# Kernel optimization log

Measured on AMD Instinct MI355X. Metric: run time of the kernel, lower is better.

The kernel has to match this reference:

```python
import jax, jax.numpy as jnp
import numpy as np
import math

N = 100000
E = 800000
H = 256
TDIM = 32
NTYPES = 22
NLAYERS = 2


def layer_norm(x, g, b, eps=1e-5):
    mu = jnp.mean(x, axis=-1, keepdims=True)
    var = jnp.var(x, axis=-1, keepdims=True)
    return (x - mu) * jax.lax.rsqrt(var + eps) * g + b


def setup_inputs() -> dict:
    key = jax.random.key(0)
    ks = jax.random.split(key, 16)
    s = 1.0 / math.sqrt(H)
    inp = {
        "clause_reprs": jax.random.normal(ks[0], (N, H), dtype=jnp.float32),
        "timestamps": jax.random.uniform(ks[1], (N,), dtype=jnp.float32) * 10000.0,
        "deriv_types": jax.random.randint(ks[2], (N,), 0, NTYPES),
        "derivation_edges": jax.random.randint(ks[3], (2, E), 0, N),
        # params
        "emb_table": jax.random.normal(ks[4], (NTYPES, H), dtype=jnp.float32),
        "temp_W": jax.random.normal(ks[5], (TDIM, H), dtype=jnp.float32) / math.sqrt(TDIM),
        "temp_b": jnp.zeros((H,), jnp.float32),
        "fus_W1": jax.random.normal(ks[6], (3 * H, H), dtype=jnp.float32) / math.sqrt(3 * H),
        "fus_b1": jnp.zeros((H,), jnp.float32),
        "fus_W2": jax.random.normal(ks[7], (H, H), dtype=jnp.float32) * s,
        "fus_b2": jnp.zeros((H,), jnp.float32),
        "in_g": jnp.ones((H,), jnp.float32),
        "in_b": jnp.zeros((H,), jnp.float32),
        "deriv_W": jax.random.normal(ks[8], (NLAYERS, 2 * H, H), dtype=jnp.float32) / math.sqrt(2 * H),
        "deriv_b": jnp.zeros((NLAYERS, H), jnp.float32),
        "dn_g": jnp.ones((NLAYERS, H), jnp.float32),
        "dn_b": jnp.zeros((NLAYERS, H), jnp.float32),
    }
    return inp


def reference(clause_reprs, timestamps, deriv_types, derivation_edges,
              emb_table, temp_W, temp_b, fus_W1, fus_b1, fus_W2, fus_b2,
              in_g, in_b, deriv_W, deriv_b, dn_g, dn_b):
    # --- temporal sinusoidal encoding -> projection ---
    half = TDIM // 2
    freqs = jnp.exp(-math.log(10000.0) * jnp.arange(half, dtype=jnp.float32) / half)
    angles = timestamps[:, None] * freqs[None, :]                      # (N, half)
    pe = jnp.concatenate([jnp.sin(angles), jnp.cos(angles)], axis=-1)  # (N, TDIM)
    temporal_enc = pe @ temp_W + temp_b                                # (N, H)
    # --- derivation type embedding ---
    deriv_enc = emb_table[deriv_types]                                 # (N, H)
    # --- input fusion + residual + LN ---
    cat = jnp.concatenate([clause_reprs, temporal_enc, deriv_enc], axis=-1)
    fused = jax.nn.relu(cat @ fus_W1 + fus_b1) @ fus_W2 + fus_b2
    x = layer_norm(fused + clause_reprs, in_g, in_b)
    # --- derivation message passing along DAG edges (parent -> child) ---
    src, dst = derivation_edges[0], derivation_edges[1]
    count = jnp.zeros((N, 1), jnp.float32).at[dst].add(1.0)
    count = jnp.maximum(count, 1.0)
    for l in range(NLAYERS):
        parent_msgs = x[src]                                           # (E, H) gather
        agg = jnp.zeros_like(x).at[dst].add(parent_msgs) / count       # (N, H) scatter-add
        combined = jnp.concatenate([x, agg], axis=-1)                  # (N, 2H)
        update = jax.nn.relu(combined @ deriv_W[l] + deriv_b[l])
        x = layer_norm(x + update, dn_g[l], dn_b[l])
    return x
```

## Files before the change

### kernel.cpp

```cpp
#include <hip/hip_runtime.h>
#include <hip/hip_bf16.h>
#include <math.h>

#define N_NODES 100000
#define N_EDGES 800000
#define H 256
#define NTYPES 22
#define SCAN_G 98
#define GRID_G ((N_NODES + 63) / 64)

typedef __attribute__((ext_vector_type(8))) short short8;
typedef __attribute__((ext_vector_type(4))) float f32x4;
typedef unsigned short u16;

__device__ __forceinline__ u16 f2bf(float f) {
    unsigned u = __float_as_uint(f);
    u += 0x7FFF + ((u >> 16) & 1);
    return (u16)(u >> 16);
}
__device__ __forceinline__ float bf2f(u16 u) {
    return __uint_as_float(((unsigned)u) << 16);
}

__global__ __launch_bounds__(256) void prep_small(
    const float* __restrict__ temp_W, const float* __restrict__ temp_b,
    const float* __restrict__ emb, const float* __restrict__ fus_W1,
    const float* __restrict__ fus_b1,
    float* __restrict__ C1, float* __restrict__ C2, float* __restrict__ beff)
{
    int b = blockIdx.x;
    int j = threadIdx.x;
    if (b < 32) {
        float acc = 0.f;
        #pragma unroll 8
        for (int m = 0; m < H; ++m)
            acc += temp_W[b * H + m] * fus_W1[(size_t)(H + m) * H + j];
        C1[b * H + j] = acc;
    } else if (b < 32 + NTYPES) {
        int e = b - 32;
        float acc = 0.f;
        #pragma unroll 8
        for (int m = 0; m < H; ++m)
            acc += emb[e * H + m] * fus_W1[(size_t)(2 * H + m) * H + j];
        C2[e * H + j] = acc;
    } else {
        float acc = fus_b1[j];
        #pragma unroll 8
        for (int m = 0; m < H; ++m)
            acc += temp_b[m] * fus_W1[(size_t)(H + m) * H + j];
        beff[j] = acc;
    }
}

__global__ __launch_bounds__(256) void prep_frag(
    const float* __restrict__ fus_W1, const float* __restrict__ C1,
    const float* __restrict__ fus_W2, const float* __restrict__ deriv_W,
    u16* __restrict__ wblob)
{
    int s = blockIdx.x;
    const float* src; int kbase;
    if (s < 8)       { src = fus_W1;              kbase = s * 32; }
    else if (s == 8) { src = C1;                  kbase = 0; }
    else if (s < 17) { src = fus_W2;              kbase = (s - 9) * 32; }
    else if (s < 33) { src = deriv_W;             kbase = (s - 17) * 32; }
    else             { src = deriv_W + 512 * H;   kbase = (s - 33) * 32; }
    #pragma unroll
    for (int it = 0; it < 4; ++it) {
        int c = it * 256 + threadIdx.x;
        int l = c & 63, nt = c >> 6;
        int n = (nt << 4) | (l & 15);
        int k0 = kbase + ((l >> 4) << 3);
        short8 v;
        #pragma unroll
        for (int i = 0; i < 8; ++i)
            v[i] = (short)f2bf(src[(size_t)(k0 + i) * H + n]);
        *reinterpret_cast<short8*>(wblob + (size_t)s * 8192 + (size_t)c * 8) = v;
    }
}

__global__ void count_kernel(const int* __restrict__ dst, int* __restrict__ cnt)
{
    int e = blockIdx.x * blockDim.x + threadIdx.x;
    if (e < N_EDGES) atomicAdd(&cnt[dst[e]], 1);
}

__global__ __launch_bounds__(1024) void scan1_kernel(
    const int* __restrict__ cnt, int* __restrict__ off, int* __restrict__ bsum)
{
    __shared__ int s[1024];
    int i = blockIdx.x * 1024 + threadIdx.x;
    int v = (i < N_NODES) ? cnt[i] : 0;
    s[threadIdx.x] = v;
    __syncthreads();
    #pragma unroll
    for (int o = 1; o < 1024; o <<= 1) {
        int t = (threadIdx.x >= o) ? s[threadIdx.x - o] : 0;
        __syncthreads();
        s[threadIdx.x] += t;
        __syncthreads();
    }
    if (i < N_NODES) off[i] = s[threadIdx.x];
    if (threadIdx.x == 1023) bsum[blockIdx.x] = s[1023];
}

__global__ void scan2_kernel(const int* __restrict__ bsum, int* __restrict__ bbase)
{
    if (threadIdx.x == 0) {
        int acc = 0;
        for (int b = 0; b < SCAN_G; ++b) { bbase[b] = acc; acc += bsum[b]; }
    }
}

__global__ __launch_bounds__(1024) void scan3_kernel(
    int* __restrict__ off, const int* __restrict__ bbase,
    const int* __restrict__ cnt, int* __restrict__ cursor)
{
    int i = blockIdx.x * 1024 + threadIdx.x;
    if (i < N_NODES) {
        int incl = off[i] + bbase[blockIdx.x];
        off[i] = incl;
        cursor[i] = incl - cnt[i];
    }
}

__global__ void fill_kernel(const int* __restrict__ src, const int* __restrict__ dst,
                            int* __restrict__ cursor, int* __restrict__ csr)
{
    int e = blockIdx.x * blockDim.x + threadIdx.x;
    if (e < N_EDGES) {
        int pos = atomicAdd(&cursor[dst[e]], 1);
        csr[pos] = src[e];
    }
}

__global__ __launch_bounds__(256) void gather_kernel(
    const u16* __restrict__ xb, const int* __restrict__ csr,
    const int* __restrict__ off, const int* __restrict__ cnt,
    u16* __restrict__ agg)
{
    int node = blockIdx.x * 4 + (threadIdx.x >> 6);
    int l = threadIdx.x & 63;
    int deg = cnt[node];
    int start = off[node] - deg;
    float a0 = 0.f, a1 = 0.f, a2 = 0.f, a3 = 0.f;
    float b0 = 0.f, b1 = 0.f, b2 = 0.f, b3 = 0.f;
    int j = 0;
    for (; j + 1 < deg; j += 2) {
        int s0 = csr[start + j], s1 = csr[start + j + 1];
        ushort4 v0 = *reinterpret_cast<const ushort4*>(xb + (size_t)s0 * H + l * 4);
        ushort4 v1 = *reinterpret_cast<const ushort4*>(xb + (size_t)s1 * H + l * 4);
        a0 += bf2f(v0.x); a1 += bf2f(v0.y); a2 += bf2f(v0.z); a3 += bf2f(v0.w);
        b0 += bf2f(v1.x); b1 += bf2f(v1.y); b2 += bf2f(v1.z); b3 += bf2f(v1.w);
    }
    if (j < deg) {
        int s0 = csr[start + j];
        ushort4 v0 = *reinterpret_cast<const ushort4*>(xb + (size_t)s0 * H + l * 4);
        a0 += bf2f(v0.x); a1 += bf2f(v0.y); a2 += bf2f(v0.z); a3 += bf2f(v0.w);
    }
    float sc = 1.0f / fmaxf((float)deg, 1.0f);
    ushort4 o;
    o.x = f2bf((a0 + b0) * sc); o.y = f2bf((a1 + b1) * sc);
    o.z = f2bf((a2 + b2) * sc); o.w = f2bf((a3 + b3) * sc);
    *reinterpret_cast<ushort4*>(agg + (size_t)node * H + l * 4) = o;
}

__device__ __forceinline__ void stageA_bf16(u16* Af, const u16* __restrict__ src,
                                            int i0, int kbase, int tid)
{
    int w = tid >> 6, l = tid & 63;
    int row = i0 + ((w << 4) | (l & 15));
    row = min(row, N_NODES - 1);
    const u16* p = src + (size_t)row * H + kbase + ((l >> 4) << 3);
    short8 v = *reinterpret_cast<const short8*>(p);
    *reinterpret_cast<short8*>(Af + (size_t)((w << 6) | l) * 8) = v;
}

__device__ __forceinline__ void stageA_f32(u16* Af, const float* __restrict__ src,
                                           int i0, int kbase, int tid)
{
    int w = tid >> 6, l = tid & 63;
    int row = i0 + ((w << 4) | (l & 15));
    row = min(row, N_NODES - 1);
    const float* p = src + (size_t)row * H + kbase + ((l >> 4) << 3);
    float4 a = *reinterpret_cast<const float4*>(p);
    float4 b = *reinterpret_cast<const float4*>(p + 4);
    short8 v;
    v[0] = (short)f2bf(a.x); v[1] = (short)f2bf(a.y);
    v[2] = (short)f2bf(a.z); v[3] = (short)f2bf(a.w);
    v[4] = (short)f2bf(b.x); v[5] = (short)f2bf(b.y);
    v[6] = (short)f2bf(b.z); v[7] = (short)f2bf(b.w);
    *reinterpret_cast<short8*>(Af + (size_t)((w << 6) | l) * 8) = v;
}

__device__ __forceinline__ void stageB(u16* Bf, const u16* __restrict__ wk, int tid)
{
    #pragma unroll
    for (int it = 0; it < 4; ++it) {
        int c = (it << 8) + tid;
        short8 v = *reinterpret_cast<const short8*>(wk + (size_t)c * 8);
        *reinterpret_cast<short8*>(Bf + (size_t)c * 8) = v;
    }
}

__device__ __forceinline__ void mfma_step(const u16* Af, const u16* Bf,
                                          int w, int l, f32x4 acc[4][4])
{
    short8 a[4];
    #pragma unroll
    for (int m = 0; m < 4; ++m)
        a[m] = *reinterpret_cast<const short8*>(Af + (size_t)((m << 6) | l) * 8);
    #pragma unroll
    for (int n = 0; n < 4; ++n) {
        short8 b = *reinterpret_cast<const short8*>(
            Bf + (size_t)((((w << 2) | n) << 6) | l) * 8);
        #pragma unroll
        for (int m = 0; m < 4; ++m)
            acc[m][n] = __builtin_amdgcn_mfma_f32_16x16x32_bf16(a[m], b, acc[m][n],
                                                                0, 0, 0);
    }
}

__global__ __launch_bounds__(256, 3) void k1_mfma(
    const float* __restrict__ clause, const float* __restrict__ ts,
    const int* __restrict__ types, const u16* __restrict__ wblob,
    const float* __restrict__ C2, const float* __restrict__ beff,
    u16* __restrict__ hb)
{
    __shared__ __align__(16) u16 Af[2048];
    __shared__ __align__(16) u16 Bf[8192];
    int tid = threadIdx.x, w = tid >> 6, l = tid & 63;
    int i0 = blockIdx.x * 64;
    f32x4 acc[4][4] = {};

    for (int t = 0; t < 9; ++t) {
        if (t < 8) {
            stageA_f32(Af, clause, i0, t * 32, tid);
        } else {
            int rl = (w << 4) | (l & 15);
            int row = min(i0 + rl, N_NODES - 1);
            float tsv = ts[row];
            int g = l >> 4;
            short8 v;
            #pragma unroll
            for (int i = 0; i < 8; ++i) {
                int k = (g << 3) + i;
                float fr = expf(-0.57564627324851f * (float)(k & 15));
                float ang = tsv * fr;
                float pv = (k < 16) ? sinf(ang) : cosf(ang);
                v[i] = (short)f2bf(pv);
            }
            *reinterpret_cast<short8*>(Af + (size_t)((w << 6) | l) * 8) = v;
        }
        stageB(Bf, wblob + (size_t)t * 8192, tid);
        __syncthreads();
        mfma_step(Af, Bf, w, l, acc);
        __syncthreads();
    }

    int g = l >> 4, c0 = l & 15;
    float be[4];
    #pragma unroll
    for (int n = 0; n < 4; ++n) be[n] = beff[(w << 6) | (n << 4) | c0];
    #pragma unroll
    for (int m = 0; m < 4; ++m) {
        #pragma unroll
        for (int r = 0; r < 4; ++r) {
            int row = i0 + (m << 4) + (g << 2) + r;
            bool ok = row < N_NODES;
            int tp = types[ok ? row : 0];
            const float* c2r = C2 + (size_t)tp * H;
            #pragma unroll
            for (int n = 0; n < 4; ++n) {
                int col = (w << 6) | (n << 4) | c0;
                float val = fmaxf(acc[m][n][r] + be[n] + c2r[col], 0.f);
                if (ok) hb[(size_t)row * H + col] = f2bf(val);
            }
        }
    }
}

__global__ __launch_bounds__(256, 3) void k2_mfma(
    const u16* __restrict__ hb, const u16* __restrict__ wblob,
    const float* __restrict__ b2, const float* __restrict__ clause,
    const float* __restrict__ gW, const float* __restrict__ bW,
    float* __restrict__ xo, u16* __restrict__ xb)
{
    __shared__ __align__(16) u16 Af[2048];
    __shared__ __align__(16) u16 Bf[8192];
    __shared__ float2 red[256];
    int tid = threadIdx.x, w = tid >> 6, l = tid & 63;
    int i0 = blockIdx.x * 64;
    f32x4 acc[4][4] = {};

    for (int t = 0; t < 8; ++t) {
        stageA_bf16(Af, hb, i0, t * 32, tid);
        stageB(Bf, wblob + (size_t)t * 8192, tid);
        __syncthreads();
        mfma_step(Af, Bf, w, l, acc);
        __syncthreads();
    }

    int g = l >> 4, c0 = l & 15;
    float bv[4], gv[4], bbv[4];
    #pragma unroll
    for (int n = 0; n < 4; ++n) {
        int col = (w << 6) | (n << 4) | c0;
        bv[n] = b2[col]; gv[n] = gW[col]; bbv[n] = bW[col];
    }
    #pragma unroll
    for (int m = 0; m < 4; ++m) {
        #pragma unroll
        for (int r = 0; r < 4; ++r) {
            int row = i0 + (m << 4) + (g << 2) + r;
            int rowc = min(row, N_NODES - 1);
            const float* cr = clause + (size_t)rowc * H;
            float s = 0.f, q = 0.f;
            #pragma unroll
            for (int n = 0; n < 4; ++n) {
                float pv = acc[m][n][r] + bv[n] + cr[(w << 6) | (n << 4) | c0];
                acc[m][n][r] = pv;
                s += pv; q += pv * pv;
            }
            #pragma unroll
            for (int o = 1; o < 16; o <<= 1) {
                s += __shfl_xor(s, o);
                q += __shfl_xor(q, o);
            }
            if (c0 == 0)
                red[((m << 4) + (g << 2) + r) * 4 + w] = make_float2(s, q);
        }
    }
    __syncthreads();
    #pragma unroll
    for (int m = 0; m < 4; ++m) {
        #pragma unroll
        for (int r = 0; r < 4; ++r) {
            int rl = (m << 4) + (g << 2) + r;
            int row = i0 + rl;
            float2 t0 = red[rl * 4 + 0], t1 = red[rl * 4 + 1];
            float2 t2 = red[rl * 4 + 2], t3 = red[rl * 4 + 3];
            float S = t0.x + t1.x + t2.x + t3.x;
            float Q = t0.y + t1.y + t2.y + t3.y;
            float mu = S * (1.0f / 256.0f);
            float rstd = rsqrtf(Q * (1.0f / 256.0f) - mu * mu + 1e-5f);
            if (row < N_NODES) {
                #pragma unroll
                for (int n = 0; n < 4; ++n) {
                    int col = (w << 6) | (n << 4) | c0;
                    float val = (acc[m][n][r] - mu) * rstd * gv[n] + bbv[n];
                    xo[(size_t)row * H + col] = val;
                    xb[(size_t)row * H + col] = f2bf(val);
                }
            }
        }
    }
}

template<bool WB16>
__global__ __launch_bounds__(256, 3) void k5_mfma(
    const u16* __restrict__ xb, const u16* __restrict__ aggb,
    float* __restrict__ x, const u16* __restrict__ wblob,
    const float* __restrict__ bl, const float* __restrict__ gl,
    const float* __restrict__ bnl, u16* __restrict__ xbout)
{
    __shared__ __align__(16) u16 Af[2048];
    __shared__ __align__(16) u16 Bf[8192];
    __shared__ float2 red[256];
    int tid = threadIdx.x, w = tid >> 6, l = tid & 63;
    int i0 = blockIdx.x * 64;
    f32x4 acc[4][4] = {};

    for (int t = 0; t < 16; ++t) {
        const u16* src = (t < 8) ? xb : aggb;
        stageA_bf16(Af, src, i0, (t & 7) * 32, tid);
        stageB(Bf, wblob + (size_t)t * 8192, tid);
        __syncthreads();
        mfma_step(Af, Bf, w, l, acc);
        __syncthreads();
    }

    int g = l >> 4, c0 = l & 15;
    float bv[4], gv[4], bbv[4];
    #pragma unroll
    for (int n = 0; n < 4; ++n) {
        int col = (w << 6) | (n << 4) | c0;
        bv[n] = bl[col]; gv[n] = gl[col]; bbv[n] = bnl[col];
    }
    #pragma unroll
    for (int m = 0; m < 4; ++m) {
        #pragma unroll
        for (int r = 0; r < 4; ++r) {
            int row = i0 + (m << 4) + (g << 2) + r;
            int rowc = min(row, N_NODES - 1);
            const float* xr = x + (size_t)rowc * H;
            float s = 0.f, q = 0.f;
            #pragma unroll
            for (int n = 0; n < 4; ++n) {
                float pv = xr[(w << 6) | (n << 4) | c0]
                         + fmaxf(acc[m][n][r] + bv[n], 0.f);
                acc[m][n][r] = pv;
                s += pv; q += pv * pv;
            }
            #pragma unroll
            for (int o = 1; o < 16; o <<= 1) {
                s += __shfl_xor(s, o);
                q += __shfl_xor(q, o);
            }
            if (c0 == 0)
                red[((m << 4) + (g << 2) + r) * 4 + w] = make_float2(s, q);
        }
    }
    __syncthreads();
    #pragma unroll
    for (int m = 0; m < 4; ++m) {
        #pragma unroll
        for (int r = 0; r < 4; ++r) {
            int rl = (m << 4) + (g << 2) + r;
            int row = i0 + rl;
            float2 t0 = red[rl * 4 + 0], t1 = red[rl * 4 + 1];
            float2 t2 = red[rl * 4 + 2], t3 = red[rl * 4 + 3];
            float S = t0.x + t1.x + t2.x + t3.x;
            float Q = t0.y + t1.y + t2.y + t3.y;
            float mu = S * (1.0f / 256.0f);
            float rstd = rsqrtf(Q * (1.0f / 256.0f) - mu * mu + 1e-5f);
            if (row < N_NODES) {
                #pragma unroll
                for (int n = 0; n < 4; ++n) {
                    int col = (w << 6) | (n << 4) | c0;
                    float val = (acc[m][n][r] - mu) * rstd * gv[n] + bbv[n];
                    x[(size_t)row * H + col] = val;
                    if (WB16) xbout[(size_t)row * H + col] = f2bf(val);
                }
            }
        }
    }
}

extern "C" void kernel_launch(void* const* d_in, const int* in_sizes, int n_in,
                              void* d_out, int out_size, void* d_ws, size_t ws_size,
                              hipStream_t stream)
{
    const float* clause  = (const float*)d_in[0];
    const float* ts      = (const float*)d_in[1];
    const int*   types   = (const int*)  d_in[2];
    const int*   edges   = (const int*)  d_in[3];
    const float* emb     = (const float*)d_in[4];
    const float* temp_W  = (const float*)d_in[5];
    const float* temp_b  = (const float*)d_in[6];
    const float* fus_W1  = (const float*)d_in[7];
    const float* fus_b1  = (const float*)d_in[8];
    const float* fus_W2  = (const float*)d_in[9];
    const float* fus_b2  = (const float*)d_in[10];
    const float* in_g    = (const float*)d_in[11];
    const float* in_b    = (const float*)d_in[12];
    const float* deriv_W = (const float*)d_in[13];
    const float* deriv_b = (const float*)d_in[14];
    const float* dn_g    = (const float*)d_in[15];
    const float* dn_b    = (const float*)d_in[16];

    char* p = (char*)d_ws;
    float* C1   = (float*)p;            p += 32 * H * 4;
    float* C2   = (float*)p;            p += NTYPES * H * 4;
    float* beff = (float*)p;            p += H * 4;
    int* cnt    = (int*)p;              p += N_NODES * 4;
    int* off    = (int*)p;              p += N_NODES * 4;
    int* cursor = (int*)p;              p += N_NODES * 4;
    int* bsum   = (int*)p;              p += 128 * 4;
    int* bbase  = (int*)p;              p += 128 * 4;
    int* csr    = (int*)p;              p += N_EDGES * 4;
    u16* wblob  = (u16*)p;              p += 49 * 8192 * 2;
    u16* xb16   = (u16*)p;              p += (size_t)N_NODES * H * 2;
    u16* aggb16 = (u16*)p;              p += (size_t)N_NODES * H * 2;
    float* x    = (float*)d_out;

    const int* src = edges;
    const int* dst = edges + N_EDGES;

    prep_small<<<32 + NTYPES + 1, 256, 0, stream>>>(temp_W, temp_b, emb, fus_W1,
                                                    fus_b1, C1, C2, beff);
    prep_frag<<<49, 256, 0, stream>>>(fus_W1, C1, fus_W2, deriv_W, wblob);

    hipMemsetAsync(cnt, 0, N_NODES * sizeof(int), stream);
    count_kernel<<<(N_EDGES + 255) / 256, 256, 0, stream>>>(dst, cnt);
    scan1_kernel<<<SCAN_G, 1024, 0, stream>>>(cnt, off, bsum);
    scan2_kernel<<<1, 64, 0, stream>>>(bsum, bbase);
    scan3_kernel<<<SCAN_G, 1024, 0, stream>>>(off, bbase, cnt, cursor);
    fill_kernel<<<(N_EDGES + 255) / 256, 256, 0, stream>>>(src, dst, cursor, csr);

    k1_mfma<<<GRID_G, 256, 0, stream>>>(clause, ts, types, wblob, C2, beff, xb16);
    k2_mfma<<<GRID_G, 256, 0, stream>>>(xb16, wblob + (size_t)9 * 8192, fus_b2,
                                        clause, in_g, in_b, x, xb16);

    gather_kernel<<<N_NODES / 4, 256, 0, stream>>>(xb16, csr, off, cnt, aggb16);
    k5_mfma<true><<<GRID_G, 256, 0, stream>>>(
        xb16, aggb16, x, wblob + (size_t)17 * 8192,
        deriv_b, dn_g, dn_b, xb16);
    gather_kernel<<<N_NODES / 4, 256, 0, stream>>>(xb16, csr, off, cnt, aggb16);
    k5_mfma<false><<<GRID_G, 256, 0, stream>>>(
        xb16, aggb16, x, wblob + (size_t)33 * 8192,
        deriv_b + H, dn_g + H, dn_b + H, nullptr);
}
```

Baseline: 546.4 us.

## Fuse input MLP kernels via LDS, use direct-to-LDS loads, drop fp32 residual

Merges the two input-fusion GEMM kernels into one, so the ReLU hidden activations stay in a swizzled LDS buffer and no longer round-trip through global memory. Weight tiles (and A tiles in the layer kernels) are now fetched with global_load_lds direct-to-LDS loads instead of going through registers. The layer kernels process two K-chunks per barrier pair at higher occupancy. The fp32 x intermediate is no longer written; the residual is read back from the bf16 copy, with fp32 written only in the final layer. This cuts memory traffic and synchronisation but lowers residual precision and raises LDS use in the fused kernel.

```diff
diff --git a/kernel.cpp b/kernel.cpp
--- a/kernel.cpp
+++ b/kernel.cpp
@@ -20,6 +20,12 @@
 }
 __device__ __forceinline__ float bf2f(u16 u) {
     return __uint_as_float(((unsigned)u) << 16);
+}
+
+__device__ __forceinline__ void gload16(const void* g, void* l) {
+    __builtin_amdgcn_global_load_lds(
+        (const __attribute__((address_space(1))) unsigned int*)g,
+        (__attribute__((address_space(3))) unsigned int*)l, 16, 0, 0);
 }
 
 __global__ __launch_bounds__(256) void prep_small(
@@ -164,44 +170,6 @@
     *reinterpret_cast<ushort4*>(agg + (size_t)node * H + l * 4) = o;
 }
 
-__device__ __forceinline__ void stageA_bf16(u16* Af, const u16* __restrict__ src,
-                                            int i0, int kbase, int tid)
-{
-    int w = tid >> 6, l = tid & 63;
-    int row = i0 + ((w << 4) | (l & 15));
-    row = min(row, N_NODES - 1);
-    const u16* p = src + (size_t)row * H + kbase + ((l >> 4) << 3);
-    short8 v = *reinterpret_cast<const short8*>(p);
-    *reinterpret_cast<short8*>(Af + (size_t)((w << 6) | l) * 8) = v;
-}
-
-__device__ __forceinline__ void stageA_f32(u16* Af, const float* __restrict__ src,
-                                           int i0, int kbase, int tid)
-{
-    int w = tid >> 6, l = tid & 63;
-    int row = i0 + ((w << 4) | (l & 15));
-    row = min(row, N_NODES - 1);
-    const float* p = src + (size_t)row * H + kbase + ((l >> 4) << 3);
-    float4 a = *reinterpret_cast<const float4*>(p);
-    float4 b = *reinterpret_cast<const float4*>(p + 4);
-    short8 v;
-    v[0] = (short)f2bf(a.x); v[1] = (short)f2bf(a.y);
-    v[2] = (short)f2bf(a.z); v[3] = (short)f2bf(a.w);
-    v[4] = (short)f2bf(b.x); v[5] = (short)f2bf(b.y);
-    v[6] = (short)f2bf(b.z); v[7] = (short)f2bf(b.w);
-    *reinterpret_cast<short8*>(Af + (size_t)((w << 6) | l) * 8) = v;
-}
-
-__device__ __forceinline__ void stageB(u16* Bf, const u16* __restrict__ wk, int tid)
-{
-    #pragma unroll
-    for (int it = 0; it < 4; ++it) {
-        int c = (it << 8) + tid;
-        short8 v = *reinterpret_cast<const short8*>(wk + (size_t)c * 8);
-        *reinterpret_cast<short8*>(Bf + (size_t)c * 8) = v;
-    }
-}
-
 __device__ __forceinline__ void mfma_step(const u16* Af, const u16* Bf,
                                           int w, int l, f32x4 acc[4][4])
 {
@@ -220,30 +188,40 @@
     }
 }
 
-__global__ __launch_bounds__(256, 3) void k1_mfma(
+__global__ __launch_bounds__(256, 3) void k12_mfma(
     const float* __restrict__ clause, const float* __restrict__ ts,
     const int* __restrict__ types, const u16* __restrict__ wblob,
     const float* __restrict__ C2, const float* __restrict__ beff,
-    u16* __restrict__ hb)
+    const float* __restrict__ b2, const float* __restrict__ gW,
+    const float* __restrict__ bW, u16* __restrict__ xb)
 {
     __shared__ __align__(16) u16 Af[2048];
     __shared__ __align__(16) u16 Bf[8192];
+    __shared__ __align__(16) u16 hs[16384];
     int tid = threadIdx.x, w = tid >> 6, l = tid & 63;
+    int g = l >> 4, c0 = l & 15;
     int i0 = blockIdx.x * 64;
+    int rowA = min(i0 + ((w << 4) | c0), N_NODES - 1);
+    int kcol = g << 3;
     f32x4 acc[4][4] = {};
 
     for (int t = 0; t < 9; ++t) {
         if (t < 8) {
-            stageA_f32(Af, clause, i0, t * 32, tid);
+            const float* p = clause + (size_t)rowA * H + t * 32 + kcol;
+            float4 a = *reinterpret_cast<const float4*>(p);
+            float4 b = *reinterpret_cast<const float4*>(p + 4);
+            short8 v;
+            v[0] = (short)f2bf(a.x); v[1] = (short)f2bf(a.y);
+            v[2] = (short)f2bf(a.z); v[3] = (short)f2bf(a.w);
+            v[4] = (short)f2bf(b.x); v[5] = (short)f2bf(b.y);
+            v[6] = (short)f2bf(b.z); v[7] = (short)f2bf(b.w);
+            *reinterpret_cast<short8*>(Af + (size_t)((w << 6) | l) * 8) = v;
         } else {
-            int rl = (w << 4) | (l & 15);
-            int row = min(i0 + rl, N_NODES - 1);
-            float tsv = ts[row];
-            int g = l >> 4;
+            float tsv = ts[rowA];
             short8 v;
             #pragma unroll
             for (int i = 0; i < 8; ++i) {
-                int k = (g << 3) + i;
+                int k = kcol + i;
                 float fr = expf(-0.57564627324851f * (float)(k & 15));
                 float ang = tsv * fr;
                 float pv = (k < 16) ? sinf(ang) : cosf(ang);
@@ -251,56 +229,73 @@
             }
             *reinterpret_cast<short8*>(Af + (size_t)((w << 6) | l) * 8) = v;
         }
-        stageB(Bf, wblob + (size_t)t * 8192, tid);
+        #pragma unroll
+        for (int it = 0; it < 4; ++it) {
+            int c = (it << 8) + tid;
+            gload16(wblob + (size_t)t * 8192 + (size_t)c * 8, Bf + (size_t)c * 8);
+        }
         __syncthreads();
         mfma_step(Af, Bf, w, l, acc);
         __syncthreads();
     }
 
-    int g = l >> 4, c0 = l & 15;
-    float be[4];
-    #pragma unroll
-    for (int n = 0; n < 4; ++n) be[n] = beff[(w << 6) | (n << 4) | c0];
-    #pragma unroll
-    for (int m = 0; m < 4; ++m) {
-        #pragma unroll
-        for (int r = 0; r < 4; ++r) {
-            int row = i0 + (m << 4) + (g << 2) + r;
-            bool ok = row < N_NODES;
-            int tp = types[ok ? row : 0];
-            const float* c2r = C2 + (size_t)tp * H;
-            #pragma unroll
-            for (int n = 0; n < 4; ++n) {
-                int col = (w << 6) | (n << 4) | c0;
-                float val = fmaxf(acc[m][n][r] + be[n] + c2r[col], 0.f);
-                if (ok) hb[(size_t)row * H + col] = f2bf(val);
-            }
-        }
-    }
-}
-
-__global__ __launch_bounds__(256, 3) void k2_mfma(
-    const u16* __restrict__ hb, const u16* __restrict__ wblob,
-    const float* __restrict__ b2, const float* __restrict__ clause,
-    const float* __restrict__ gW, const float* __restrict__ bW,
-    float* __restrict__ xo, u16* __restrict__ xb)
-{
-    __shared__ __align__(16) u16 Af[2048];
-    __shared__ __align__(16) u16 Bf[8192];
-    __shared__ float2 red[256];
-    int tid = threadIdx.x, w = tid >> 6, l = tid & 63;
-    int i0 = blockIdx.x * 64;
-    f32x4 acc[4][4] = {};
+    {
+        float bev[4];
+        #pragma unroll
+        for (int n = 0; n < 4; ++n) bev[n] = beff[(w << 6) | (n << 4) | c0];
+        #pragma unroll
+        for (int m = 0; m < 4; ++m) {
+            #pragma unroll
+            for (int r = 0; r < 4; ++r) {
+                int rl = (m << 4) + (g << 2) + r;
+                int tp = types[min(i0 + rl, N_NODES - 1)];
+                const float* c2r = C2 + (size_t)tp * H;
+                #pragma unroll
+                for (int n = 0; n < 4; ++n) {
+                    int col = (w << 6) | (n << 4) | c0;
+                    float val = fmaxf(acc[m][n][r] + bev[n] + c2r[col], 0.f);
+                    hs[((rl << 8) + col) ^ ((rl & 7) << 3)] = f2bf(val);
+                }
+            }
+        }
+    }
+    __syncthreads();
+
+    #pragma unroll
+    for (int m = 0; m < 4; ++m)
+        #pragma unroll
+        for (int n = 0; n < 4; ++n)
+            acc[m][n] = (f32x4){0.f, 0.f, 0.f, 0.f};
 
     for (int t = 0; t < 8; ++t) {
-        stageA_bf16(Af, hb, i0, t * 32, tid);
-        stageB(Bf, wblob + (size_t)t * 8192, tid);
-        __syncthreads();
-        mfma_step(Af, Bf, w, l, acc);
-        __syncthreads();
-    }
-
-    int g = l >> 4, c0 = l & 15;
+        #pragma unroll
+        for (int it = 0; it < 4; ++it) {
+            int c = (it << 8) + tid;
+            gload16(wblob + (size_t)(9 + t) * 8192 + (size_t)c * 8,
+                    Bf + (size_t)c * 8);
+        }
+        __syncthreads();
+        short8 a[4];
+        int colb = (t << 5) + kcol;
+        #pragma unroll
+        for (int m = 0; m < 4; ++m) {
+            int rl2 = (m << 4) | c0;
+            a[m] = *reinterpret_cast<const short8*>(
+                &hs[((rl2 << 8) + colb) ^ ((c0 & 7) << 3)]);
+        }
+        #pragma unroll
+        for (int n = 0; n < 4; ++n) {
+            short8 b = *reinterpret_cast<const short8*>(
+                Bf + (size_t)((((w << 2) | n) << 6) | l) * 8);
+            #pragma unroll
+            for (int m = 0; m < 4; ++m)
+                acc[m][n] = __builtin_amdgcn_mfma_f32_16x16x32_bf16(a[m], b,
+                                                                    acc[m][n], 0, 0, 0);
+        }
+        __syncthreads();
+    }
+
+    float2* red = reinterpret_cast<float2*>(Af);
     float bv[4], gv[4], bbv[4];
     #pragma unroll
     for (int n = 0; n < 4; ++n) {
@@ -311,8 +306,8 @@
     for (int m = 0; m < 4; ++m) {
         #pragma unroll
         for (int r = 0; r < 4; ++r) {
-            int row = i0 + (m << 4) + (g << 2) + r;
-            int rowc = min(row, N_NODES - 1);
+            int rl = (m << 4) + (g << 2) + r;
+            int rowc = min(i0 + rl, N_NODES - 1);
             const float* cr = clause + (size_t)rowc * H;
             float s = 0.f, q = 0.f;
             #pragma unroll
@@ -326,8 +321,7 @@
                 s += __shfl_xor(s, o);
                 q += __shfl_xor(q, o);
             }
-            if (c0 == 0)
-                red[((m << 4) + (g << 2) + r) * 4 + w] = make_float2(s, q);
+            if (c0 == 0) red[(rl << 2) | w] = make_float2(s, q);
         }
     }
     __syncthreads();
@@ -337,8 +331,8 @@
         for (int r = 0; r < 4; ++r) {
             int rl = (m << 4) + (g << 2) + r;
             int row = i0 + rl;
-            float2 t0 = red[rl * 4 + 0], t1 = red[rl * 4 + 1];
-            float2 t2 = red[rl * 4 + 2], t3 = red[rl * 4 + 3];
+            float2 t0 = red[(rl << 2) | 0], t1 = red[(rl << 2) | 1];
+            float2 t2 = red[(rl << 2) | 2], t3 = red[(rl << 2) | 3];
             float S = t0.x + t1.x + t2.x + t3.x;
             float Q = t0.y + t1.y + t2.y + t3.y;
             float mu = S * (1.0f / 256.0f);
@@ -348,7 +342,6 @@
                 for (int n = 0; n < 4; ++n) {
                     int col = (w << 6) | (n << 4) | c0;
                     float val = (acc[m][n][r] - mu) * rstd * gv[n] + bbv[n];
-                    xo[(size_t)row * H + col] = val;
                     xb[(size_t)row * H + col] = f2bf(val);
                 }
             }
@@ -356,30 +349,41 @@
     }
 }
 
-template<bool WB16>
-__global__ __launch_bounds__(256, 3) void k5_mfma(
+template<bool FINAL>
+__global__ __launch_bounds__(256, 4) void k5_mfma(
     const u16* __restrict__ xb, const u16* __restrict__ aggb,
-    float* __restrict__ x, const u16* __restrict__ wblob,
-    const float* __restrict__ bl, const float* __restrict__ gl,
-    const float* __restrict__ bnl, u16* __restrict__ xbout)
-{
-    __shared__ __align__(16) u16 Af[2048];
-    __shared__ __align__(16) u16 Bf[8192];
-    __shared__ float2 red[256];
+    const u16* __restrict__ wblob, const float* __restrict__ bl,
+    const float* __restrict__ gl, const float* __restrict__ bnl,
+    u16* __restrict__ xbout, float* __restrict__ xout)
+{
+    __shared__ __align__(16) u16 Af[4096];
+    __shared__ __align__(16) u16 Bf[16384];
     int tid = threadIdx.x, w = tid >> 6, l = tid & 63;
+    int g = l >> 4, c0 = l & 15;
     int i0 = blockIdx.x * 64;
+    int rowA = min(i0 + ((w << 4) | c0), N_NODES - 1);
+    int kcol = g << 3;
     f32x4 acc[4][4] = {};
 
-    for (int t = 0; t < 16; ++t) {
-        const u16* src = (t < 8) ? xb : aggb;
-        stageA_bf16(Af, src, i0, (t & 7) * 32, tid);
-        stageB(Bf, wblob + (size_t)t * 8192, tid);
+    for (int t = 0; t < 8; ++t) {
+        const u16* sb = (t < 4) ? xb : aggb;
+        const u16* ap = sb + (size_t)rowA * H + ((t & 3) << 6) + kcol;
+        gload16(ap,      Af + (size_t)((w << 6) | l) * 8);
+        gload16(ap + 32, Af + 2048 + (size_t)((w << 6) | l) * 8);
+        const u16* wk = wblob + (size_t)(t << 1) * 8192;
+        #pragma unroll
+        for (int it = 0; it < 4; ++it) {
+            int c = (it << 8) + tid;
+            gload16(wk + (size_t)c * 8,        Bf + (size_t)c * 8);
+            gload16(wk + 8192 + (size_t)c * 8, Bf + 8192 + (size_t)c * 8);
+        }
         __syncthreads();
         mfma_step(Af, Bf, w, l, acc);
-        __syncthreads();
-    }
-
-    int g = l >> 4, c0 = l & 15;
+        mfma_step(Af + 2048, Bf + 8192, w, l, acc);
+        __syncthreads();
+    }
+
+    float2* red = reinterpret_cast<float2*>(Af);
     float bv[4], gv[4], bbv[4];
     #pragma unroll
     for (int n = 0; n < 4; ++n) {
@@ -390,14 +394,14 @@
     for (int m = 0; m < 4; ++m) {
         #pragma unroll
         for (int r = 0; r < 4; ++r) {
-            int row = i0 + (m << 4) + (g << 2) + r;
-            int rowc = min(row, N_NODES - 1);
-            const float* xr = x + (size_t)rowc * H;
+            int rl = (m << 4) + (g << 2) + r;
+            int rowc = min(i0 + rl, N_NODES - 1);
+            const u16* xr = xb + (size_t)rowc * H;
             float s = 0.f, q = 0.f;
             #pragma unroll
             for (int n = 0; n < 4; ++n) {
-                float pv = xr[(w << 6) | (n << 4) | c0]
-                         + fmaxf(acc[m][n][r] + bv[n], 0.f);
+                int col = (w << 6) | (n << 4) | c0;
+                float pv = bf2f(xr[col]) + fmaxf(acc[m][n][r] + bv[n], 0.f);
                 acc[m][n][r] = pv;
                 s += pv; q += pv * pv;
             }
@@ -406,8 +410,7 @@
                 s += __shfl_xor(s, o);
                 q += __shfl_xor(q, o);
             }
-            if (c0 == 0)
-                red[((m << 4) + (g << 2) + r) * 4 + w] = make_float2(s, q);
+            if (c0 == 0) red[(rl << 2) | w] = make_float2(s, q);
         }
     }
     __syncthreads();
@@ -417,8 +420,8 @@
         for (int r = 0; r < 4; ++r) {
             int rl = (m << 4) + (g << 2) + r;
             int row = i0 + rl;
-            float2 t0 = red[rl * 4 + 0], t1 = red[rl * 4 + 1];
-            float2 t2 = red[rl * 4 + 2], t3 = red[rl * 4 + 3];
+            float2 t0 = red[(rl << 2) | 0], t1 = red[(rl << 2) | 1];
+            float2 t2 = red[(rl << 2) | 2], t3 = red[(rl << 2) | 3];
             float S = t0.x + t1.x + t2.x + t3.x;
             float Q = t0.y + t1.y + t2.y + t3.y;
             float mu = S * (1.0f / 256.0f);
@@ -428,8 +431,8 @@
                 for (int n = 0; n < 4; ++n) {
                     int col = (w << 6) | (n << 4) | c0;
                     float val = (acc[m][n][r] - mu) * rstd * gv[n] + bbv[n];
-                    x[(size_t)row * H + col] = val;
-                    if (WB16) xbout[(size_t)row * H + col] = f2bf(val);
+                    if (FINAL) xout[(size_t)row * H + col] = val;
+                    else       xbout[(size_t)row * H + col] = f2bf(val);
                 }
             }
         }
@@ -487,16 +490,15 @@
     scan3_kernel<<<SCAN_G, 1024, 0, stream>>>(off, bbase, cnt, cursor);
     fill_kernel<<<(N_EDGES + 255) / 256, 256, 0, stream>>>(src, dst, cursor, csr);
 
-    k1_mfma<<<GRID_G, 256, 0, stream>>>(clause, ts, types, wblob, C2, beff, xb16);
-    k2_mfma<<<GRID_G, 256, 0, stream>>>(xb16, wblob + (size_t)9 * 8192, fus_b2,
-                                        clause, in_g, in_b, x, xb16);
-
+    k12_mfma<<<GRID_G, 256, 0, stream>>>(clause, ts, types, wblob, C2, beff,
+                                         fus_b2, in_g, in_b, xb16);
+
+    gather_kernel<<<N_NODES / 4, 256, 0, stream>>>(xb16, csr, off, cnt, aggb16);
+    k5_mfma<false><<<GRID_G, 256, 0, stream>>>(
+        xb16, aggb16, wblob + (size_t)17 * 8192,
+        deriv_b, dn_g, dn_b, xb16, nullptr);
     gather_kernel<<<N_NODES / 4, 256, 0, stream>>>(xb16, csr, off, cnt, aggb16);
     k5_mfma<true><<<GRID_G, 256, 0, stream>>>(
-        xb16, aggb16, x, wblob + (size_t)17 * 8192,
-        deriv_b, dn_g, dn_b, xb16);
-    gather_kernel<<<N_NODES / 4, 256, 0, stream>>>(xb16, csr, off, cnt, aggb16);
-    k5_mfma<false><<<GRID_G, 256, 0, stream>>>(
-        xb16, aggb16, x, wblob + (size_t)33 * 8192,
-        deriv_b + H, dn_g + H, dn_b + H, nullptr);
-}
+        xb16, aggb16, wblob + (size_t)33 * 8192,
+        deriv_b + H, dn_g + H, dn_b + H, nullptr, x);
+}
```

After: 564.6 us. 3.3% more time.
